# Optimization experiments

Hardware: AMD Instinct MI355X
Metric: run time of the kernel (lower is better)

Reference implementation:

```python
import jax, jax.numpy as jnp
import numpy as np

B, C, N, K = 4, 192, 8192, 16
C_OUT = 192


def _gather_nodes(xs, idx):
    # xs: [B, C, N], idx: [B, N, K] -> [B, C, N, K]
    return jax.vmap(lambda xb, ib: xb[:, ib])(xs, idx)


def setup_inputs() -> dict:
    key = jax.random.key(0)
    k1, k2, k3 = jax.random.split(key, 3)
    x = jax.random.normal(k1, (B, C, N, 1), dtype=jnp.float32)
    x_0 = jnp.zeros((B, C, N, 1), dtype=jnp.float32)  # unused by forward, kept for interface
    edge_index = jax.random.randint(k2, (2, B, N, K), 0, N, dtype=jnp.int32)
    # 1x1 Conv2d(2C -> C_OUT) weight flattened to [C_OUT, 2C]
    W = jax.random.normal(k3, (C_OUT, 2 * C), dtype=jnp.float32) / np.sqrt(2 * C)
    b = jnp.zeros((C_OUT,), dtype=jnp.float32)
    return {"x": x, "x_0": x_0, "edge_index": edge_index, "W": W, "b": b}


def reference(x, x_0, edge_index, W, b):
    xs = x[..., 0]                       # [B, C, N]
    x_i = _gather_nodes(xs, edge_index[1])   # centers  [B, C, N, K]
    x_j = _gather_nodes(xs, edge_index[0])   # neighbors [B, C, N, K]
    rel = jnp.max(x_j - x_i, axis=-1)        # max-relative [B, C, N]
    y = jnp.concatenate([xs, rel], axis=1)   # [B, 2C, N]
    out = jnp.einsum('oc,bcn->bon', W, y) + b[None, :, None]  # 1x1 conv
    out = jax.nn.relu(out)
    return out[..., None]                # [B, C_OUT, N, 1]
```

## Files before the change

### kernel.cpp

```cpp
#include <hip/hip_runtime.h>

#define B_    4
#define C_    192
#define N_    8192
#define K_    16
#define O_    192
#define TWOC_ 384

typedef __attribute__((ext_vector_type(8))) short short8;
typedef __attribute__((ext_vector_type(4))) short short4v;
typedef __attribute__((ext_vector_type(2))) unsigned int uint2v;
typedef __attribute__((ext_vector_type(4))) float floatx4;

static __device__ __forceinline__ float bf2f(unsigned int u16) {
    union { unsigned int i; float f; } v; v.i = u16 << 16; return v.f;
}
static __device__ __forceinline__ unsigned short f2bf(float f) {
    union { float f; unsigned int i; } v; v.f = f;
    unsigned int x = v.i;
    return (unsigned short)((x + 0x7FFFu + ((x >> 16) & 1u)) >> 16);
}

__global__ __launch_bounds__(256) void k_convert_w(const float* __restrict__ W,
                                                   unsigned short* __restrict__ Wb) {
    int i = blockIdx.x * 256 + threadIdx.x;
    if (i < O_ * TWOC_) Wb[i] = f2bf(W[i]);
}

__global__ __launch_bounds__(256) void k_transpose(const float* __restrict__ x,
                                                   unsigned short* __restrict__ xt) {
    __shared__ float tile[32][33];
    int bid  = blockIdx.x;
    int xcd  = bid & 7;
    int b    = xcd >> 1;
    int half = xcd & 1;
    int slot = bid >> 3;
    int ct   = slot >> 7;
    int nt   = half * 128 + (slot & 127);
    int c0 = ct * 32, n0 = nt * 32;
    int tid = threadIdx.x;

    int cc  = tid >> 3;
    int nn4 = (tid & 7) * 4;
    const float* xp = x + ((size_t)b * C_ + c0 + cc) * N_ + n0 + nn4;
    float4 v = *(const float4*)xp;
    tile[nn4 + 0][cc] = v.x;
    tile[nn4 + 1][cc] = v.y;
    tile[nn4 + 2][cc] = v.z;
    tile[nn4 + 3][cc] = v.w;
    __syncthreads();

#pragma unroll
    for (int i = 0; i < 2; i++) {
        int id  = i * 256 + tid;
        int row = id >> 4;
        int ch2 = id & 15;
        float a = tile[row][ch2 * 2];
        float c = tile[row][ch2 * 2 + 1];
        unsigned int pack = (unsigned int)f2bf(a) | ((unsigned int)f2bf(c) << 16);
        *(unsigned int*)(xt + ((size_t)b * N_ + n0 + row) * C_ + c0 + ch2 * 2) = pack;
    }
}

__global__ __launch_bounds__(256) void k_fused(const unsigned short* __restrict__ xt,
                                               const int* __restrict__ eidx,
                                               const unsigned short* __restrict__ Wb,
                                               const float* __restrict__ bias,
                                               float* __restrict__ out) {
    __shared__ unsigned short ytile[64][TWOC_];
    __shared__ int sidx[64][33];

    int bid  = blockIdx.x;
    int xcd  = bid & 7;
    int b    = xcd >> 1;
    int slot = bid >> 3;
    int n0   = ((xcd & 1) * 64 + slot) * 64;

    int tid  = threadIdx.x;
    int wave = tid >> 6;
    int lane = tid & 63;

    const int* e0 = eidx + ((size_t)b * N_ + n0) * K_;
    const int* e1 = e0 + (size_t)B_ * N_ * K_;
#pragma unroll
    for (int i = 0; i < 4; i++) {
        int id   = i * 256 + tid;
        int node = id >> 4, k = id & 15;
        sidx[node][k]      = e0[id];
        sidx[node][16 + k] = e1[id];
    }

    const unsigned short* xrow = xt + ((size_t)b * N_ + n0) * C_;
#pragma unroll
    for (int i = 0; i < 6; i++) {
        int id = i * 256 + tid;
        int row = id / 24, chunk = id % 24;
        short8 v = *(const short8*)(xrow + (size_t)row * C_ + chunk * 8);
        *(short8*)&ytile[row][chunk * 8] = v;
    }
    __syncthreads();

    {
        int g  = lane >> 4;
        int l4 = lane & 15;
        const unsigned short* xbase = xt + (size_t)b * N_ * C_;
#pragma unroll
        for (int bb = 0; bb < 4; bb++) {
            int node = wave * 16 + bb * 4 + g;
            float m[3][4];
#pragma unroll
            for (int t = 0; t < 3; t++)
#pragma unroll
                for (int c = 0; c < 4; c++) m[t][c] = -INFINITY;
#pragma unroll
            for (int k = 0; k < K_; k++) {
                int jn = sidx[node][k];
                int in = sidx[node][16 + k];
                const unsigned short* pj = xbase + (size_t)jn * C_ + l4 * 4;
                const unsigned short* pi = xbase + (size_t)in * C_ + l4 * 4;
#pragma unroll
                for (int t = 0; t < 3; t++) {
                    uint2v vj = *(const uint2v*)(pj + t * 64);
                    uint2v vi = *(const uint2v*)(pi + t * 64);
                    m[t][0] = fmaxf(m[t][0], bf2f(vj.x & 0xffffu) - bf2f(vi.x & 0xffffu));
                    m[t][1] = fmaxf(m[t][1], bf2f(vj.x >> 16)     - bf2f(vi.x >> 16));
                    m[t][2] = fmaxf(m[t][2], bf2f(vj.y & 0xffffu) - bf2f(vi.y & 0xffffu));
                    m[t][3] = fmaxf(m[t][3], bf2f(vj.y >> 16)     - bf2f(vi.y >> 16));
                }
            }
#pragma unroll
            for (int t = 0; t < 3; t++) {
                short4v s;
                s.x = (short)f2bf(m[t][0]);
                s.y = (short)f2bf(m[t][1]);
                s.z = (short)f2bf(m[t][2]);
                s.w = (short)f2bf(m[t][3]);
                *(short4v*)&ytile[node][C_ + t * 64 + l4 * 4] = s;
            }
        }
    }
    __syncthreads();

    int m16  = lane & 15;
    int quad = lane >> 4;
    const unsigned short* wbase = Wb + (size_t)(wave * 48 + m16) * TWOC_ + quad * 8;

    floatx4 acc[3][4];
#pragma unroll
    for (int i = 0; i < 3; i++)
#pragma unroll
        for (int j = 0; j < 4; j++) acc[i][j] = (floatx4){0.f, 0.f, 0.f, 0.f};

#pragma unroll 2
    for (int kt = 0; kt < 12; kt++) {
        short8 wf[3], yf[4];
#pragma unroll
        for (int i = 0; i < 3; i++)
            wf[i] = *(const short8*)(wbase + (size_t)(i * 16) * TWOC_ + kt * 32);
#pragma unroll
        for (int j = 0; j < 4; j++)
            yf[j] = *(const short8*)&ytile[j * 16 + m16][kt * 32 + quad * 8];
#pragma unroll
        for (int i = 0; i < 3; i++)
#pragma unroll
            for (int j = 0; j < 4; j++)
                acc[i][j] = __builtin_amdgcn_mfma_f32_16x16x32_bf16(wf[i], yf[j], acc[i][j], 0, 0, 0);
    }

#pragma unroll
    for (int i = 0; i < 3; i++) {
#pragma unroll
        for (int r = 0; r < 4; r++) {
            int o = wave * 48 + i * 16 + quad * 4 + r;
            float bv = bias[o];
#pragma unroll
            for (int j = 0; j < 4; j++) {
                int n = n0 + j * 16 + m16;
                out[((size_t)b * O_ + o) * N_ + n] = fmaxf(acc[i][j][r] + bv, 0.f);
            }
        }
    }
}

extern "C" void kernel_launch(void* const* d_in, const int* in_sizes, int n_in,
                              void* d_out, int out_size, void* d_ws, size_t ws_size,
                              hipStream_t stream) {
    const float* x    = (const float*)d_in[0];
    const int*   eidx = (const int*)d_in[2];
    const float* W    = (const float*)d_in[3];
    const float* bias = (const float*)d_in[4];
    float*       out  = (float*)d_out;

    unsigned short* Wb = (unsigned short*)d_ws;
    unsigned short* xt = (unsigned short*)((char*)d_ws + 147456);

    k_convert_w<<<dim3((O_ * TWOC_ + 255) / 256), dim3(256), 0, stream>>>(W, Wb);
    k_transpose<<<dim3(6144), dim3(256), 0, stream>>>(x, xt);
    k_fused<<<dim3(512), dim3(256), 0, stream>>>(xt, eidx, Wb, bias, out);
}
```

Before: 136.0 us.

## Halve fused tile to 32 nodes, prefetch gathers, merge prep kernels

Merges the weight conversion and transpose kernels into one launch. Halves the node tile in the fused kernel to 32, doubling the grid to 1024 blocks, and pads the LDS rows to 392 to avoid bank conflicts. Adds a min-occupancy hint to launch bounds. The neighbor gather loop now double-buffers its loads so the next neighbor is fetched while the current one is reduced, and the bf16 high-half extraction uses a mask instead of a shift. Smaller tiles reuse each weight fragment across fewer nodes, so weight reads from L2 go up, while the extra buffers add register pressure.

New measurement: 141.6 us. +4.1%, slower.

```diff
diff --git a/kernel.cpp b/kernel.cpp
--- a/kernel.cpp
+++ b/kernel.cpp
@@ -6,14 +6,18 @@
 #define K_    16
 #define O_    192
 #define TWOC_ 384
+#define YPAD  392
 
 typedef __attribute__((ext_vector_type(8))) short short8;
 typedef __attribute__((ext_vector_type(4))) short short4v;
 typedef __attribute__((ext_vector_type(2))) unsigned int uint2v;
 typedef __attribute__((ext_vector_type(4))) float floatx4;
 
-static __device__ __forceinline__ float bf2f(unsigned int u16) {
-    union { unsigned int i; float f; } v; v.i = u16 << 16; return v.f;
+static __device__ __forceinline__ float bf_lo(unsigned int u) {
+    union { unsigned int i; float f; } v; v.i = u << 16; return v.f;
+}
+static __device__ __forceinline__ float bf_hi(unsigned int u) {
+    union { unsigned int i; float f; } v; v.i = u & 0xffff0000u; return v.f;
 }
 static __device__ __forceinline__ unsigned short f2bf(float f) {
     union { float f; unsigned int i; } v; v.f = f;
@@ -21,16 +25,17 @@
     return (unsigned short)((x + 0x7FFFu + ((x >> 16) & 1u)) >> 16);
 }
 
-__global__ __launch_bounds__(256) void k_convert_w(const float* __restrict__ W,
-                                                   unsigned short* __restrict__ Wb) {
-    int i = blockIdx.x * 256 + threadIdx.x;
-    if (i < O_ * TWOC_) Wb[i] = f2bf(W[i]);
-}
-
-__global__ __launch_bounds__(256) void k_transpose(const float* __restrict__ x,
-                                                   unsigned short* __restrict__ xt) {
+__global__ __launch_bounds__(256) void k_prep(const float* __restrict__ x,
+                                              const float* __restrict__ W,
+                                              unsigned short* __restrict__ xt,
+                                              unsigned short* __restrict__ Wb) {
+    int bid = blockIdx.x;
+    if (bid >= 6144) {
+        int i = (bid - 6144) * 256 + threadIdx.x;
+        if (i < O_ * TWOC_) Wb[i] = f2bf(W[i]);
+        return;
+    }
     __shared__ float tile[32][33];
-    int bid  = blockIdx.x;
     int xcd  = bid & 7;
     int b    = xcd >> 1;
     int half = xcd & 1;
@@ -62,19 +67,19 @@
     }
 }
 
-__global__ __launch_bounds__(256) void k_fused(const unsigned short* __restrict__ xt,
-                                               const int* __restrict__ eidx,
-                                               const unsigned short* __restrict__ Wb,
-                                               const float* __restrict__ bias,
-                                               float* __restrict__ out) {
-    __shared__ unsigned short ytile[64][TWOC_];
-    __shared__ int sidx[64][33];
+__global__ __launch_bounds__(256, 4) void k_fused(const unsigned short* __restrict__ xt,
+                                                  const int* __restrict__ eidx,
+                                                  const unsigned short* __restrict__ Wb,
+                                                  const float* __restrict__ bias,
+                                                  float* __restrict__ out) {
+    __shared__ unsigned short ytile[32][YPAD];
+    __shared__ int sidx[32][33];
 
     int bid  = blockIdx.x;
     int xcd  = bid & 7;
     int b    = xcd >> 1;
     int slot = bid >> 3;
-    int n0   = ((xcd & 1) * 64 + slot) * 64;
+    int n0   = ((xcd & 1) * 128 + slot) * 32;
 
     int tid  = threadIdx.x;
     int wave = tid >> 6;
@@ -83,8 +88,8 @@
     const int* e0 = eidx + ((size_t)b * N_ + n0) * K_;
     const int* e1 = e0 + (size_t)B_ * N_ * K_;
 #pragma unroll
-    for (int i = 0; i < 4; i++) {
-        int id   = i * 256 + tid;
+    for (int i = 0; i < 2; i++) {
+        int id = i * 256 + tid;
         int node = id >> 4, k = id & 15;
         sidx[node][k]      = e0[id];
         sidx[node][16 + k] = e1[id];
@@ -92,7 +97,7 @@
 
     const unsigned short* xrow = xt + ((size_t)b * N_ + n0) * C_;
 #pragma unroll
-    for (int i = 0; i < 6; i++) {
+    for (int i = 0; i < 3; i++) {
         int id = i * 256 + tid;
         int row = id / 24, chunk = id % 24;
         short8 v = *(const short8*)(xrow + (size_t)row * C_ + chunk * 8);
@@ -105,27 +110,45 @@
         int l4 = lane & 15;
         const unsigned short* xbase = xt + (size_t)b * N_ * C_;
 #pragma unroll
-        for (int bb = 0; bb < 4; bb++) {
-            int node = wave * 16 + bb * 4 + g;
-            float m[3][4];
-#pragma unroll
-            for (int t = 0; t < 3; t++)
-#pragma unroll
-                for (int c = 0; c < 4; c++) m[t][c] = -INFINITY;
-#pragma unroll
-            for (int k = 0; k < K_; k++) {
-                int jn = sidx[node][k];
-                int in = sidx[node][16 + k];
+        for (int bb = 0; bb < 2; bb++) {
+            int node = wave * 8 + bb * 4 + g;
+            uint2v bj[2][3], bi[2][3];
+            {
+                int jn = sidx[node][0], in = sidx[node][16];
                 const unsigned short* pj = xbase + (size_t)jn * C_ + l4 * 4;
                 const unsigned short* pi = xbase + (size_t)in * C_ + l4 * 4;
 #pragma unroll
                 for (int t = 0; t < 3; t++) {
-                    uint2v vj = *(const uint2v*)(pj + t * 64);
-                    uint2v vi = *(const uint2v*)(pi + t * 64);
-                    m[t][0] = fmaxf(m[t][0], bf2f(vj.x & 0xffffu) - bf2f(vi.x & 0xffffu));
-                    m[t][1] = fmaxf(m[t][1], bf2f(vj.x >> 16)     - bf2f(vi.x >> 16));
-                    m[t][2] = fmaxf(m[t][2], bf2f(vj.y & 0xffffu) - bf2f(vi.y & 0xffffu));
-                    m[t][3] = fmaxf(m[t][3], bf2f(vj.y >> 16)     - bf2f(vi.y >> 16));
+                    bj[0][t] = *(const uint2v*)(pj + t * 64);
+                    bi[0][t] = *(const uint2v*)(pi + t * 64);
+                }
+            }
+            float m[3][4];
+#pragma unroll
+            for (int t = 0; t < 3; t++)
+#pragma unroll
+                for (int c = 0; c < 4; c++) m[t][c] = -INFINITY;
+
+#pragma unroll
+            for (int k = 0; k < K_; k++) {
+                int cur = k & 1, nxt = cur ^ 1;
+                if (k < K_ - 1) {
+                    int jn = sidx[node][k + 1], in = sidx[node][16 + k + 1];
+                    const unsigned short* pj = xbase + (size_t)jn * C_ + l4 * 4;
+                    const unsigned short* pi = xbase + (size_t)in * C_ + l4 * 4;
+#pragma unroll
+                    for (int t = 0; t < 3; t++) {
+                        bj[nxt][t] = *(const uint2v*)(pj + t * 64);
+                        bi[nxt][t] = *(const uint2v*)(pi + t * 64);
+                    }
+                }
+#pragma unroll
+                for (int t = 0; t < 3; t++) {
+                    uint2v vj = bj[cur][t], vi = bi[cur][t];
+                    m[t][0] = fmaxf(m[t][0], bf_lo(vj.x) - bf_lo(vi.x));
+                    m[t][1] = fmaxf(m[t][1], bf_hi(vj.x) - bf_hi(vi.x));
+                    m[t][2] = fmaxf(m[t][2], bf_lo(vj.y) - bf_lo(vi.y));
+                    m[t][3] = fmaxf(m[t][3], bf_hi(vj.y) - bf_hi(vi.y));
                 }
             }
 #pragma unroll
@@ -145,25 +168,25 @@
     int quad = lane >> 4;
     const unsigned short* wbase = Wb + (size_t)(wave * 48 + m16) * TWOC_ + quad * 8;
 
-    floatx4 acc[3][4];
+    floatx4 acc[3][2];
 #pragma unroll
     for (int i = 0; i < 3; i++)
 #pragma unroll
-        for (int j = 0; j < 4; j++) acc[i][j] = (floatx4){0.f, 0.f, 0.f, 0.f};
-
-#pragma unroll 2
+        for (int j = 0; j < 2; j++) acc[i][j] = (floatx4){0.f, 0.f, 0.f, 0.f};
+
+#pragma unroll
     for (int kt = 0; kt < 12; kt++) {
-        short8 wf[3], yf[4];
+        short8 wf[3], yf[2];
 #pragma unroll
         for (int i = 0; i < 3; i++)
             wf[i] = *(const short8*)(wbase + (size_t)(i * 16) * TWOC_ + kt * 32);
 #pragma unroll
-        for (int j = 0; j < 4; j++)
+        for (int j = 0; j < 2; j++)
             yf[j] = *(const short8*)&ytile[j * 16 + m16][kt * 32 + quad * 8];
 #pragma unroll
         for (int i = 0; i < 3; i++)
 #pragma unroll
-            for (int j = 0; j < 4; j++)
+            for (int j = 0; j < 2; j++)
                 acc[i][j] = __builtin_amdgcn_mfma_f32_16x16x32_bf16(wf[i], yf[j], acc[i][j], 0, 0, 0);
     }
 
@@ -174,7 +197,7 @@
             int o = wave * 48 + i * 16 + quad * 4 + r;
             float bv = bias[o];
 #pragma unroll
-            for (int j = 0; j < 4; j++) {
+            for (int j = 0; j < 2; j++) {
                 int n = n0 + j * 16 + m16;
                 out[((size_t)b * O_ + o) * N_ + n] = fmaxf(acc[i][j][r] + bv, 0.f);
             }
@@ -194,7 +217,6 @@
     unsigned short* Wb = (unsigned short*)d_ws;
     unsigned short* xt = (unsigned short*)((char*)d_ws + 147456);
 
-    k_convert_w<<<dim3((O_ * TWOC_ + 255) / 256), dim3(256), 0, stream>>>(W, Wb);
-    k_transpose<<<dim3(6144), dim3(256), 0, stream>>>(x, xt);
-    k_fused<<<dim3(512), dim3(256), 0, stream>>>(xt, eidx, Wb, bias, out);
-}
+    k_prep<<<dim3(6144 + 288), dim3(256), 0, stream>>>(x, W, xt, Wb);
+    k_fused<<<dim3(1024), dim3(256), 0, stream>>>(xt, eidx, Wb, bias, out);
+}
```

## Split fused gather+GEMM into separate gather and GEMM kernels with prefetching

Applied to the files above, without the earlier changes.

Splits the fused kernel into two. k_gather uses small blocks of 16 nodes for higher occupancy, software-pipelines the neighbour row loads with a three-slot register buffer, and writes the max-relative features to a workspace buffer. k_gemm uses single-wave blocks that read W, xt and rel straight from global memory, with no LDS staging, and compute 64x64 output tiles with MFMA. This removes the low-occupancy fused kernel, where gather latency was poorly hidden, but adds an extra global round trip for rel and an extra kernel launch.

New measurement: 223.1 us. 64.0% more time.

```diff
diff --git a/kernel.cpp b/kernel.cpp
--- a/kernel.cpp
+++ b/kernel.cpp
@@ -12,8 +12,11 @@
 typedef __attribute__((ext_vector_type(2))) unsigned int uint2v;
 typedef __attribute__((ext_vector_type(4))) float floatx4;
 
-static __device__ __forceinline__ float bf2f(unsigned int u16) {
-    union { unsigned int i; float f; } v; v.i = u16 << 16; return v.f;
+static __device__ __forceinline__ float bf_lo(unsigned int u) {
+    union { unsigned int i; float f; } v; v.i = u << 16; return v.f;
+}
+static __device__ __forceinline__ float bf_hi(unsigned int u) {
+    union { unsigned int i; float f; } v; v.i = u & 0xffff0000u; return v.f;
 }
 static __device__ __forceinline__ unsigned short f2bf(float f) {
     union { float f; unsigned int i; } v; v.f = f;
@@ -62,116 +65,137 @@
     }
 }
 
-__global__ __launch_bounds__(256) void k_fused(const unsigned short* __restrict__ xt,
-                                               const int* __restrict__ eidx,
-                                               const unsigned short* __restrict__ Wb,
-                                               const float* __restrict__ bias,
-                                               float* __restrict__ out) {
-    __shared__ unsigned short ytile[64][TWOC_];
-    __shared__ int sidx[64][33];
+__global__ __launch_bounds__(256, 8) void k_gather(const unsigned short* __restrict__ xt,
+                                                   const int* __restrict__ eidx,
+                                                   unsigned short* __restrict__ rel) {
+    __shared__ int sidx[16][36];
 
     int bid  = blockIdx.x;
     int xcd  = bid & 7;
     int b    = xcd >> 1;
     int slot = bid >> 3;
-    int n0   = ((xcd & 1) * 64 + slot) * 64;
+    int n0   = ((xcd & 1) * 256 + slot) * 16;
 
     int tid  = threadIdx.x;
     int wave = tid >> 6;
     int lane = tid & 63;
 
-    const int* e0 = eidx + ((size_t)b * N_ + n0) * K_;
-    const int* e1 = e0 + (size_t)B_ * N_ * K_;
-#pragma unroll
-    for (int i = 0; i < 4; i++) {
-        int id   = i * 256 + tid;
-        int node = id >> 4, k = id & 15;
-        sidx[node][k]      = e0[id];
-        sidx[node][16 + k] = e1[id];
-    }
-
-    const unsigned short* xrow = xt + ((size_t)b * N_ + n0) * C_;
-#pragma unroll
-    for (int i = 0; i < 6; i++) {
-        int id = i * 256 + tid;
-        int row = id / 24, chunk = id % 24;
-        short8 v = *(const short8*)(xrow + (size_t)row * C_ + chunk * 8);
-        *(short8*)&ytile[row][chunk * 8] = v;
+    {
+        const int* e0 = eidx + ((size_t)b * N_ + n0) * K_;
+        const int* e1 = e0 + (size_t)B_ * N_ * K_;
+        int node = tid >> 4, k = tid & 15;
+        sidx[node][k]      = e0[tid];
+        sidx[node][16 + k] = e1[tid];
     }
     __syncthreads();
 
-    {
-        int g  = lane >> 4;
-        int l4 = lane & 15;
-        const unsigned short* xbase = xt + (size_t)b * N_ * C_;
-#pragma unroll
-        for (int bb = 0; bb < 4; bb++) {
-            int node = wave * 16 + bb * 4 + g;
-            float m[3][4];
-#pragma unroll
-            for (int t = 0; t < 3; t++)
-#pragma unroll
-                for (int c = 0; c < 4; c++) m[t][c] = -INFINITY;
-#pragma unroll
-            for (int k = 0; k < K_; k++) {
-                int jn = sidx[node][k];
-                int in = sidx[node][16 + k];
-                const unsigned short* pj = xbase + (size_t)jn * C_ + l4 * 4;
-                const unsigned short* pi = xbase + (size_t)in * C_ + l4 * 4;
-#pragma unroll
-                for (int t = 0; t < 3; t++) {
-                    uint2v vj = *(const uint2v*)(pj + t * 64);
-                    uint2v vi = *(const uint2v*)(pi + t * 64);
-                    m[t][0] = fmaxf(m[t][0], bf2f(vj.x & 0xffffu) - bf2f(vi.x & 0xffffu));
-                    m[t][1] = fmaxf(m[t][1], bf2f(vj.x >> 16)     - bf2f(vi.x >> 16));
-                    m[t][2] = fmaxf(m[t][2], bf2f(vj.y & 0xffffu) - bf2f(vi.y & 0xffffu));
-                    m[t][3] = fmaxf(m[t][3], bf2f(vj.y >> 16)     - bf2f(vi.y >> 16));
-                }
-            }
-#pragma unroll
-            for (int t = 0; t < 3; t++) {
-                short4v s;
-                s.x = (short)f2bf(m[t][0]);
-                s.y = (short)f2bf(m[t][1]);
-                s.z = (short)f2bf(m[t][2]);
-                s.w = (short)f2bf(m[t][3]);
-                *(short4v*)&ytile[node][C_ + t * 64 + l4 * 4] = s;
-            }
+    int g  = lane >> 4;
+    int l4 = lane & 15;
+    int node = wave * 4 + g;
+    const unsigned short* xbase = xt + (size_t)b * N_ * C_;
+
+#define GLD(BUF, JN, IN)                                                    \
+    {                                                                       \
+        const unsigned short* pj = xbase + (size_t)(JN) * C_ + l4 * 4;      \
+        const unsigned short* pi = xbase + (size_t)(IN) * C_ + l4 * 4;      \
+        bj[BUF][0] = *(const uint2v*)(pj);                                  \
+        bi[BUF][0] = *(const uint2v*)(pi);                                  \
+        bj[BUF][1] = *(const uint2v*)(pj + 64);                             \
+        bi[BUF][1] = *(const uint2v*)(pi + 64);                             \
+        bj[BUF][2] = *(const uint2v*)(pj + 128);                            \
+        bi[BUF][2] = *(const uint2v*)(pi + 128);                            \
+    }
+
+    uint2v bj[3][3], bi[3][3];
+    GLD(0, sidx[node][0], sidx[node][16]);
+    GLD(1, sidx[node][1], sidx[node][17]);
+
+    float m[3][4];
+#pragma unroll
+    for (int t = 0; t < 3; t++)
+#pragma unroll
+        for (int c = 0; c < 4; c++) m[t][c] = -INFINITY;
+
+#pragma unroll
+    for (int k = 0; k < K_; k++) {
+        int cb = k % 3;
+        if (k + 2 < K_) {
+            int pb = (k + 2) % 3;
+            GLD(pb, sidx[node][k + 2], sidx[node][16 + k + 2]);
         }
-    }
-    __syncthreads();
-
+#pragma unroll
+        for (int t = 0; t < 3; t++) {
+            uint2v vj = bj[cb][t], vi = bi[cb][t];
+            m[t][0] = fmaxf(m[t][0], bf_lo(vj.x) - bf_lo(vi.x));
+            m[t][1] = fmaxf(m[t][1], bf_hi(vj.x) - bf_hi(vi.x));
+            m[t][2] = fmaxf(m[t][2], bf_lo(vj.y) - bf_lo(vi.y));
+            m[t][3] = fmaxf(m[t][3], bf_hi(vj.y) - bf_hi(vi.y));
+        }
+    }
+#undef GLD
+
+    unsigned short* w = rel + ((size_t)b * N_ + n0 + node) * C_;
+#pragma unroll
+    for (int t = 0; t < 3; t++) {
+        short4v s;
+        s.x = (short)f2bf(m[t][0]);
+        s.y = (short)f2bf(m[t][1]);
+        s.z = (short)f2bf(m[t][2]);
+        s.w = (short)f2bf(m[t][3]);
+        *(short4v*)(w + t * 64 + l4 * 4) = s;
+    }
+}
+
+__global__ __launch_bounds__(64) void k_gemm(const unsigned short* __restrict__ Wb,
+                                             const unsigned short* __restrict__ xt,
+                                             const unsigned short* __restrict__ rel,
+                                             const float* __restrict__ bias,
+                                             float* __restrict__ out) {
+    int bid  = blockIdx.x;
+    int xcd  = bid & 7;
+    int b    = xcd >> 1;
+    int rest = bid >> 3;
+    int ob   = rest / 64;
+    int ns   = rest % 64;
+    int n0   = ((xcd & 1) * 64 + ns) * 64;
+
+    int lane = threadIdx.x;
     int m16  = lane & 15;
     int quad = lane >> 4;
-    const unsigned short* wbase = Wb + (size_t)(wave * 48 + m16) * TWOC_ + quad * 8;
-
-    floatx4 acc[3][4];
-#pragma unroll
-    for (int i = 0; i < 3; i++)
+
+    const unsigned short* wbase = Wb + (size_t)(ob * 64 + m16) * TWOC_ + quad * 8;
+    const unsigned short* xrow  = xt  + ((size_t)b * N_ + n0 + m16) * C_ + quad * 8;
+    const unsigned short* rrow  = rel + ((size_t)b * N_ + n0 + m16) * C_ + quad * 8;
+
+    floatx4 acc[4][4];
+#pragma unroll
+    for (int i = 0; i < 4; i++)
 #pragma unroll
         for (int j = 0; j < 4; j++) acc[i][j] = (floatx4){0.f, 0.f, 0.f, 0.f};
 
-#pragma unroll 2
+#pragma unroll
     for (int kt = 0; kt < 12; kt++) {
-        short8 wf[3], yf[4];
-#pragma unroll
-        for (int i = 0; i < 3; i++)
-            wf[i] = *(const short8*)(wbase + (size_t)(i * 16) * TWOC_ + kt * 32);
-#pragma unroll
-        for (int j = 0; j < 4; j++)
-            yf[j] = *(const short8*)&ytile[j * 16 + m16][kt * 32 + quad * 8];
-#pragma unroll
-        for (int i = 0; i < 3; i++)
+        const unsigned short* ybase = (kt < 6) ? xrow : rrow;
+        int ko = (kt < 6) ? kt * 32 : (kt - 6) * 32;
+        short8 af[4], yf[4];
+#pragma unroll
+        for (int t = 0; t < 4; t++)
+            af[t] = *(const short8*)(wbase + (size_t)(t * 16) * TWOC_ + kt * 32);
+#pragma unroll
+        for (int t = 0; t < 4; t++)
+            yf[t] = *(const short8*)(ybase + (size_t)(t * 16) * C_ + ko);
+#pragma unroll
+        for (int i = 0; i < 4; i++)
 #pragma unroll
             for (int j = 0; j < 4; j++)
-                acc[i][j] = __builtin_amdgcn_mfma_f32_16x16x32_bf16(wf[i], yf[j], acc[i][j], 0, 0, 0);
-    }
-
-#pragma unroll
-    for (int i = 0; i < 3; i++) {
+                acc[i][j] = __builtin_amdgcn_mfma_f32_16x16x32_bf16(af[i], yf[j], acc[i][j], 0, 0, 0);
+    }
+
+#pragma unroll
+    for (int i = 0; i < 4; i++) {
 #pragma unroll
         for (int r = 0; r < 4; r++) {
-            int o = wave * 48 + i * 16 + quad * 4 + r;
+            int o = ob * 64 + i * 16 + quad * 4 + r;
             float bv = bias[o];
 #pragma unroll
             for (int j = 0; j < 4; j++) {
@@ -191,10 +215,12 @@
     const float* bias = (const float*)d_in[4];
     float*       out  = (float*)d_out;
 
-    unsigned short* Wb = (unsigned short*)d_ws;
-    unsigned short* xt = (unsigned short*)((char*)d_ws + 147456);
-
-    k_convert_w<<<dim3((O_ * TWOC_ + 255) / 256), dim3(256), 0, stream>>>(W, Wb);
+    unsigned short* Wb  = (unsigned short*)d_ws;
+    unsigned short* xt  = (unsigned short*)((char*)d_ws + 147456);
+    unsigned short* rel = (unsigned short*)((char*)d_ws + 147456 + (size_t)B_ * N_ * C_ * 2);
+
+    k_convert_w<<<dim3(288), dim3(256), 0, stream>>>(W, Wb);
     k_transpose<<<dim3(6144), dim3(256), 0, stream>>>(x, xt);
-    k_fused<<<dim3(512), dim3(256), 0, stream>>>(xt, eidx, Wb, bias, out);
-}
+    k_gather<<<dim3(2048), dim3(256), 0, stream>>>(xt, eidx, rel);
+    k_gemm<<<dim3(1536), dim3(64), 0, stream>>>(Wb, xt, rel, bias, out);
+}
```
